# Optimization experiments

Hardware: AMD Instinct MI355X
Metric: run time of the kernel (lower is better)

## Reference

```python
import jax, jax.numpy as jnp
import numpy as np

N, E = 50000, 800000        # nodes, edges
L, MUL, S = 2, 32, 5        # layers, irrep multiplicity, num_species
NB, H = 8, 64               # num_bessel, radial MLP hidden
R_MAX = 5.0
AVG_NEIGH = 16.0
NW = 4 * MUL                # radial-MLP output size: 4 uvu TP paths x mul


def _envelope(x, p=6):
    # polynomial cutoff envelope u(x), smoothly -> 0 at x=1
    u = (1.0
         - (p + 1.0) * (p + 2.0) / 2.0 * x ** p
         + p * (p + 2.0) * x ** (p + 1)
         - p * (p + 1.0) / 2.0 * x ** (p + 2))
    return u * (x < 1.0)


def _forward(edge_vectors, node_species, senders, receivers, embed_w,
             w_res_s, w_res_v, w_lin1_s, w_lin1_v, mlp_w0, mlp_w1, mlp_w2,
             w_lin2_s, w_lin2_v, w_out1, w_out2):
    r = jnp.sqrt(jnp.sum(edge_vectors ** 2, -1) + 1e-12)            # [E] safe_norm
    unit = edge_vectors / r[:, None]
    sh1 = jnp.sqrt(3.0) * unit                                      # l=1 SH, component norm [E,3]
    # Bessel radial basis * polynomial envelope -> edge embedding [E,NB]
    n = jnp.arange(1, NB + 1, dtype=jnp.float32)
    bessel = jnp.sqrt(2.0 / R_MAX) * jnp.sin(n[None, :] * jnp.pi * r[:, None] / R_MAX) / r[:, None]
    edge_embedded = bessel * _envelope(r / R_MAX)[:, None]

    onehot = jax.nn.one_hot(node_species, S, dtype=jnp.float32)     # [N,S] node attrs (Sx0e)
    h_s = (onehot @ embed_w) / jnp.sqrt(S)                          # [N,MUL] 0e features
    h_v = jnp.zeros((N, MUL, 3), jnp.float32)                       # [N,MUL,3] 1o features (no path from 0e attrs)

    for l in range(L):
        # residual: FullyConnectedTensorProduct(node_feats, node_attrs) into h_out irreps
        res_s = jnp.einsum('nu,ns,usk->nk', h_s, onehot, w_res_s[l]) / jnp.sqrt(MUL * S)   # [N,2*MUL] (feat+gate scalars)
        res_v = jnp.einsum('nui,ns,usv->nvi', h_v, onehot, w_res_v[l]) / jnp.sqrt(MUL * S) # [N,MUL,3]
        # self-interaction Linear (per-irrep channel mixing)
        hs = (h_s @ w_lin1_s[l]) / jnp.sqrt(MUL)
        hv = jnp.einsum('nui,uv->nvi', h_v, w_lin1_v[l]) / jnp.sqrt(MUL)
        # gather sender node features onto edges
        es, ev = hs[senders], hv[senders]                           # [E,MUL], [E,MUL,3]
        # radial MLP (swish, no bias) -> per-edge uvu TP path weights [E, 4*MUL]
        a = jax.nn.silu(edge_embedded @ (mlp_w0[l] / jnp.sqrt(NB)))
        a = jax.nn.silu(a @ (mlp_w1[l] / jnp.sqrt(H)))
        w = a @ mlp_w2[l]
        w1, w2, w3, w4 = jnp.split(w, 4, axis=-1)
        # per-edge Clebsch-Gordan tensor product, uvu mode, radial weights
        o0a = w1 * es                                               # 0e x 0e -> 0e
        o0b = w2 * jnp.einsum('eui,ei->eu', ev, sh1) / jnp.sqrt(3.0)  # 1o x 1o -> 0e
        o1a = (w3 * es)[:, :, None] * sh1[:, None, :]               # 0e x 1o -> 1o
        o1b = w4[:, :, None] * ev                                   # 1o x 0e -> 1o
        # scatter-sum to receiver nodes + neighbor normalization
        seg = lambda x: jax.ops.segment_sum(x, receivers, num_segments=N) / AVG_NEIGH
        n0 = jnp.concatenate([seg(o0a), seg(o0b)], axis=-1)         # [N,2*MUL]
        n1 = jnp.concatenate([seg(o1a), seg(o1b)], axis=1)          # [N,2*MUL,3]
        # Linear to h_out irreps, add residual
        s_out = n0 @ w_lin2_s[l] / jnp.sqrt(2 * MUL) + res_s        # [N,2*MUL]
        v_out = jnp.einsum('nui,uv->nvi', n1, w_lin2_v[l]) / jnp.sqrt(2 * MUL) + res_v
        # gated nonlinearity: swish on even scalars, swish-activated gates scale vectors
        h_s = jax.nn.silu(s_out[:, :MUL])
        h_v = v_out * jax.nn.silu(s_out[:, MUL:])[:, :, None]
    # scalar readout: MUL -> MUL//2 -> 1 per node
    z = (h_s @ w_out1) / jnp.sqrt(MUL)
    e_node = (z @ w_out2) / jnp.sqrt(MUL // 2)
    return jnp.ravel(e_node)                                        # [N]


def setup_inputs():
    key = jax.random.key(0)
    ks = jax.random.split(key, 16)
    return {
        "edge_vectors": jax.random.normal(ks[0], (E, 3), jnp.float32) * 2.0,
        "node_species": jax.random.randint(ks[1], (N,), 0, S),
        "senders": jax.random.randint(ks[2], (E,), 0, N),
        "receivers": jax.random.randint(ks[3], (E,), 0, N),
        "embed_w": jax.random.normal(ks[4], (S, MUL), jnp.float32),
        "w_res_s": jax.random.normal(ks[5], (L, MUL, S, 2 * MUL), jnp.float32),
        "w_res_v": jax.random.normal(ks[6], (L, MUL, S, MUL), jnp.float32),
        "w_lin1_s": jax.random.normal(ks[7], (L, MUL, MUL), jnp.float32),
        "w_lin1_v": jax.random.normal(ks[8], (L, MUL, MUL), jnp.float32),
        "mlp_w0": jax.random.normal(ks[9], (L, NB, H), jnp.float32) * 4.0,
        "mlp_w1": jax.random.normal(ks[10], (L, H, H), jnp.float32) * 4.0,
        "mlp_w2": jax.random.normal(ks[11], (L, H, NW), jnp.float32) * 4.0 / np.sqrt(H),
        "w_lin2_s": jax.random.normal(ks[12], (L, 2 * MUL, 2 * MUL), jnp.float32),
        "w_lin2_v": jax.random.normal(ks[13], (L, 2 * MUL, MUL), jnp.float32),
        "w_out1": jax.random.normal(ks[14], (MUL, MUL // 2), jnp.float32),
        "w_out2": jax.random.normal(ks[15], (MUL // 2, 1), jnp.float32),
    }


def reference(edge_vectors, node_species, senders, receivers, embed_w,
              w_res_s, w_res_v, w_lin1_s, w_lin1_v, mlp_w0, mlp_w1, mlp_w2,
              w_lin2_s, w_lin2_v, w_out1, w_out2):
    return _forward(edge_vectors, node_species, senders, receivers, embed_w,
                    w_res_s, w_res_v, w_lin1_s, w_lin1_v, mlp_w0, mlp_w1, mlp_w2,
                    w_lin2_s, w_lin2_v, w_out1, w_out2)
```

## Files before the change

### kernel.cpp

```cpp
#include <hip/hip_runtime.h>
#include <math.h>

#define NN 50000
#define EE 800000
#define TB 4096

typedef float f32x2 __attribute__((ext_vector_type(2)));
typedef float f32x4  __attribute__((ext_vector_type(4)));

__device__ __forceinline__ float silu_f(float x) {
    return x / (1.f + __expf(-x));
}

__global__ __launch_bounds__(256) void k_table(
        const float* __restrict__ mlp_w0, const float* __restrict__ mlp_w1,
        const float* __restrict__ mlp_w2,
        const float* __restrict__ embed_w, const float* __restrict__ w_lin1_s,
        float* __restrict__ tab0, float* __restrict__ tab1, float* __restrict__ fs) {
    __shared__ float stage[4][128];
    int wv = threadIdx.x >> 6, lane = threadIdx.x & 63;
    int wid = blockIdx.x * 4 + wv;
    int widc = wid > 2 * TB + 1 ? 2 * TB + 1 : wid;
    int l = widc / (TB + 1);
    int bin = widc - l * (TB + 1);
    float* st = stage[wv];

    float r = 5.f * (float)bin / (float)TB;
    if (r < 1e-6f) r = 1e-6f;
    float ir = 1.f / r;
    float xx = r * 0.2f;
    float env = 0.f;
    if (xx < 1.f) {
        float x2 = xx * xx, x3 = x2 * xx, x6 = x3 * x3, x7 = x6 * xx, x8 = x7 * xx;
        env = 1.f - 28.f * x6 + 48.f * x7 - 21.f * x8;
    }
    float coef = 0.6324555320336759f * env * ir;
    const float w5 = 0.6283185307179586f;

    float p = 0.f;
#pragma unroll
    for (int k = 0; k < 8; ++k)
        p += coef * __sinf(w5 * (float)(k + 1) * r) * mlp_w0[l * 512 + k * 64 + lane];
    float a1 = silu_f(p * 0.35355339059327373f);
    st[lane] = a1;
    __syncthreads();
    float q = 0.f;
    for (int j = 0; j < 64; ++j) q += st[j] * mlp_w1[l * 4096 + j * 64 + lane];
    float a2 = silu_f(q * 0.125f);
    __syncthreads();
    st[lane] = a2;
    __syncthreads();
    float wlo = 0.f, whi = 0.f;
    for (int h = 0; h < 64; ++h) {
        float a = st[h];
        wlo += a * mlp_w2[l * 8192 + h * 128 + lane];
        whi += a * mlp_w2[l * 8192 + h * 128 + 64 + lane];
    }
    __syncthreads();
    st[lane] = wlo;
    st[64 + lane] = whi;
    __syncthreads();
    if (wid <= 2 * TB + 1 && lane < 16) {
        f32x4 o;
        if (l == 0) {
            o[0] = st[lane]; o[1] = st[64 + lane];
            o[2] = st[16 + lane]; o[3] = st[80 + lane];
            ((f32x4*)tab0)[bin * 16 + lane] = o;
        } else {
            o[0] = st[lane]; o[1] = st[32 + lane];
            o[2] = st[16 + lane]; o[3] = st[48 + lane];
            ((f32x4*)tab1)[bin * 16 + lane] = o;
        }
    }
    int ft = (wid - (2 * TB + 2)) * 64 + lane;
    if (wid >= 2 * TB + 2 && ft < 160) {
        int sp = ft >> 5, v = ft & 31;
        float acc = 0.f;
#pragma unroll
        for (int u = 0; u < 32; ++u) acc += embed_w[sp * 32 + u] * w_lin1_s[u * 32 + v];
        fs[ft] = acc * 0.4472135954999579f * 0.17677669529663687f;
    }
}

__global__ void k_hist(const int* __restrict__ recv, int* __restrict__ deg) {
    int e = blockIdx.x * 256 + threadIdx.x;
    if (e < EE) atomicAdd(&deg[recv[e]], 1);
}

__global__ void k_scan(const int* __restrict__ deg, int* __restrict__ row_start,
                       int* __restrict__ cursor) {
    __shared__ int part[256];
    int t = threadIdx.x;
    int lo = t * 196, hi = lo + 196 > NN ? NN : lo + 196;
    int s = 0;
    if (t < 255) {
        const int4* d4 = (const int4*)(deg + lo);
#pragma unroll 7
        for (int i = 0; i < 49; ++i) { int4 v = d4[i]; s += v.x + v.y + v.z + v.w; }
    } else {
        for (int i = lo; i < hi; ++i) s += deg[i];
    }
    part[t] = s;
    __syncthreads();
    for (int d = 1; d < 256; d <<= 1) {
        int add = (t >= d) ? part[t - d] : 0;
        __syncthreads();
        part[t] += add;
        __syncthreads();
    }
    int run = part[t] - s;
    for (int i = lo; i < hi; ++i) {
        row_start[i] = run;
        cursor[i] = run;
        run += deg[i];
    }
    if (t == 255) row_start[NN] = run;
}

__global__ void k_fill(const int* __restrict__ recv, const int* __restrict__ senders,
                       const int* __restrict__ species, const float* __restrict__ evec,
                       int* __restrict__ cursor,
                       int* __restrict__ csr_send, int* __restrict__ csr_recv,
                       float* __restrict__ ev4) {
    int e = blockIdx.x * 256 + threadIdx.x;
    if (e >= EE) return;
    int rv = recv[e];
    int p = atomicAdd(&cursor[rv], 1);
    int snd = senders[e];
    csr_send[p] = snd | (species[snd] << 24);
    csr_recv[p] = rv;
    float x = evec[e * 3 + 0], y = evec[e * 3 + 1], z = evec[e * 3 + 2];
    float r = sqrtf(x * x + y * y + z * z + 1e-12f);
    float ir = 1.f / r;
    const float s3 = 1.7320508075688772f;
    float xb = r * ((float)TB / 5.f);
    if (xb > (float)TB) xb = (float)TB;
    f32x4 o;
    o[0] = s3 * x * ir;
    o[1] = s3 * y * ir;
    o[2] = s3 * z * ir;
    o[3] = xb;
    *(f32x4*)(ev4 + (size_t)p * 4) = o;
}

#define WROWS 18
#define WSTRIDE 256
template<int L>
__global__ __launch_bounds__(256) void k_mega(
    const int* __restrict__ csr_send, const int* __restrict__ csr_recv,
    const float* __restrict__ ev4, const int* __restrict__ row_start,
    const float* __restrict__ fs, const float* __restrict__ feat,
    const float* __restrict__ tab,
    float* __restrict__ n0, float* __restrict__ n1) {
    __shared__ f32x4 accw4[WROWS * WSTRIDE / 4];
    __shared__ f32x4 lds_esh[256];
    __shared__ float lds_x[256];
    __shared__ int lds_wd[256];
    __shared__ int sh_base, sh_last;
    float* accw = (float*)accw4;

    int tid = threadIdx.x;
    int p0 = blockIdx.x * 256;
    int lane = tid & 63;
    int wv = tid >> 6;
    int c0 = lane & 15;
    int rg = lane >> 4;

    for (int i = tid; i < WROWS * WSTRIDE / 4; i += 256) accw4[i] = (f32x4)0.f;

    int sndp = csr_send[p0 + tid];
    int rv = csr_recv[p0 + tid];
    if (tid == 0)   sh_base = rv;
    if (tid == 255) sh_last = rv;
    {
        f32x4 g = *(const f32x4*)(ev4 + (size_t)(p0 + tid) * 4);
        f32x4 esh;
        esh[0] = g[0]; esh[1] = g[1]; esh[2] = g[2];
        esh[3] = __int_as_float(sndp);
        lds_esh[tid] = esh;
        lds_x[tid] = g[3];
    }
    __syncthreads();
    int node_base = sh_base;
    lds_wd[tid] = rv - node_base;

    const f32x4* tabv = (const f32x4*)tab;
    const f32x4* feat4 = (const f32x4*)feat;
    const float rs3 = 0.5773502691896258f;

    for (int t = 0; t < 4; ++t) {
        int tOff = wv * 64 + t * 16;

        f32x4 eshv[4], dv[4];
        int wr[4];
        float es0[4], es1[4];
#pragma unroll
        for (int j = 0; j < 4; ++j) {
            int idx = tOff + rg * 4 + j;
            eshv[j] = lds_esh[idx];
            wr[j] = lds_wd[idx];
            float xb = lds_x[idx];
            int bin = (int)xb;
            if (bin >= TB) bin = TB - 1;
            float fr = xb - (float)bin;
            f32x4 lo = tabv[bin * 16 + c0];
            f32x4 hi = tabv[bin * 16 + 16 + c0];
            dv[j] = lo + fr * (hi - lo);
            if (L == 0) {
                int sp = ((unsigned)__float_as_int(eshv[j][3])) >> 24;
                es0[j] = fs[sp * 32 + c0];
                es1[j] = fs[sp * 32 + 16 + c0];
            }
        }

#pragma unroll
        for (int b = 0; b < 2; ++b) {
            int u = b * 16 + c0;
            float s0 = 0.f, s1 = 0.f, s2 = 0.f, s3v = 0.f;
            int curw = wr[0];
            auto emit = [&](int wrow) {
                if (L == 0) {
                    if (wrow < WROWS) {
                        float* arow = accw + wrow * WSTRIDE;
                        atomicAdd(arow + u, s0);
                        atomicAdd(arow + 64 + u, s1);
                        atomicAdd(arow + 128 + u, s2);
                        atomicAdd(arow + 192 + u, s3v);
                    } else {
                        int rvn = node_base + wrow;
                        atomicAdd(n0 + (size_t)rvn * 64 + u, s0);
                        atomicAdd(n1 + (size_t)rvn * 192 + u, s1);
                        atomicAdd(n1 + (size_t)rvn * 192 + 64 + u, s2);
                        atomicAdd(n1 + (size_t)rvn * 192 + 128 + u, s3v);
                    }
                } else {
                    if (wrow < WROWS) {
                        float* arow = accw + wrow * WSTRIDE;
                        atomicAdd(arow + u, s0);
                        atomicAdd(arow + 32 + u, s1);
                    } else {
                        int rvn = node_base + wrow;
                        atomicAdd(n0 + (size_t)rvn * 64 + u, s0);
                        atomicAdd(n0 + (size_t)rvn * 64 + 32 + u, s1);
                    }
                }
            };
#pragma unroll
            for (int j = 0; j < 4; ++j) {
                int wrow = wr[j];
                if (j > 0 && wrow != curw) {
                    emit(curw);
                    s0 = s1 = s2 = s3v = 0.f;
                    curw = wrow;
                }
                f32x4 esh = eshv[j];
                float dA = dv[j][2 * b];
                float dB = dv[j][2 * b + 1];
                if (L == 0) {
                    float es = b ? es1[j] : es0[j];
                    float t3 = dB * es;
                    s0  += dA * es;
                    s1  += t3 * esh[0];
                    s2  += t3 * esh[1];
                    s3v += t3 * esh[2];
                } else {
                    int s = __float_as_int(esh[3]) & 0xFFFFFF;
                    f32x4 f4 = feat4[(size_t)s * 32 + u];
                    float dot = f4[1] * esh[0] + f4[2] * esh[1] + f4[3] * esh[2];
                    s0 += dA * f4[0];
                    s1 += dB * dot * rs3;
                }
            }
            {
                int pw = __shfl_xor(curw, 16);
                float t0 = __shfl_xor(s0, 16), t1 = __shfl_xor(s1, 16);
                float t2 = 0.f, t3m = 0.f;
                if (L == 0) { t2 = __shfl_xor(s2, 16); t3m = __shfl_xor(s3v, 16); }
                bool alive = true;
                if (pw == curw) {
                    s0 += t0; s1 += t1;
                    if (L == 0) { s2 += t2; s3v += t3m; }
                    if (lane & 16) alive = false;
                }
                if (alive) emit(curw);
            }
        }
    }
    __syncthreads();

    int span = sh_last - node_base;
    if (span > WROWS - 1) span = WROWS - 1;
    for (int wl = 0; wl <= span; ++wl) {
        int n = node_base + wl;
        float v = accw[wl * WSTRIDE + tid];
        bool interior = (row_start[n] >= p0) && (row_start[n + 1] <= p0 + 256);
        if (L == 1) {
            if (tid < 64) {
                float* dest = n0 + (size_t)n * 64 + tid;
                if (interior) *dest = v;
                else if (v != 0.f) atomicAdd(dest, v);
            }
        } else {
            float* dest = (tid < 64) ? (n0 + (size_t)n * 64 + tid) : (n1 + (size_t)n * 192 + (tid - 64));
            if (interior) *dest = v;
            else if (v != 0.f) atomicAdd(dest, v);
        }
    }
}

__global__ __launch_bounds__(256) void k_upd0_prep(
        const int* __restrict__ species,
        const float* __restrict__ n0, const float* __restrict__ n1,
        const float* __restrict__ w_lin2_s, const float* __restrict__ w_lin2_v,
        const float* __restrict__ w_res_s, const float* __restrict__ embed_w,
        const float* __restrict__ w_lin1_s, const float* __restrict__ w_lin1_v,
        float* __restrict__ h_s, float* __restrict__ feat) {
    __shared__ float stage[4][128];
    int lane = threadIdx.x & 63;
    int wv = threadIdx.x >> 6;
    int n = blockIdx.x * 4 + wv;
    n = __builtin_amdgcn_readfirstlane(n);
    int sp = __builtin_amdgcn_readfirstlane(species[n]);
    const float sc_l2 = 1.f / 128.f;
    const float rr = 0.07905694150420949f * 0.4472135954999579f;

    const float* n0r = n0 + (size_t)n * 64;
    float sk = 0.f;
#pragma unroll 8
    for (int j = 0; j < 64; ++j)
        sk += n0r[j] * w_lin2_s[j * 64 + lane];
    sk *= sc_l2;
#pragma unroll 8
    for (int u = 0; u < 32; ++u)
        sk += (embed_w[sp * 32 + u] * rr) * w_res_s[(u * 5 + sp) * 64 + lane];
    float act = silu_f(sk);
    float gmine = __shfl(act, 32 + (lane & 31));

    const float* n1r = n1 + (size_t)n * 192;
    int i0 = lane >> 5, v = lane & 31;
    float acc0 = 0.f, acc2 = 0.f;
#pragma unroll 8
    for (int u = 0; u < 32; ++u) {
        float wlv = w_lin2_v[u * 32 + v];
        acc0 += n1r[i0 * 64 + u] * wlv;
        acc2 += n1r[128 + u] * wlv;
    }
    float* st = stage[wv];
    st[32 + i0 * 32 + v] = acc0 * sc_l2 * gmine;
    if (lane < 32) {
        st[v] = act;
        st[96 + v] = acc2 * sc_l2 * gmine;
        h_s[(size_t)n * 32 + v] = act;
    }
    __syncthreads();

    const float rs32 = 0.17677669529663687f;
    float accA = 0.f, accB = 0.f;
#pragma unroll 8
    for (int u = 0; u < 32; ++u) {
        float wsv = w_lin1_s[u * 32 + v];
        float wvv = w_lin1_v[u * 32 + v];
        float xs = st[u];
        float xx = st[32 + u];
        float xy = st[64 + u];
        float xz = st[96 + u];
        float inA = i0 ? xy : xs;
        float wA  = i0 ? wvv : wsv;
        float inB = i0 ? xz : xx;
        accA += inA * wA;
        accB += inB * wvv;
    }
    f32x2 o;
    o[0] = accA * rs32;
    o[1] = accB * rs32;
    *(f32x2*)(feat + (size_t)n * 128 + v * 4 + i0 * 2) = o;
}

__global__ __launch_bounds__(256) void k_node_update_last(
        const int* __restrict__ species,
        const float* __restrict__ n0,
        const float* __restrict__ w_lin2_s, const float* __restrict__ w_res_s,
        const float* __restrict__ h_s,
        const float* __restrict__ w_out1, const float* __restrict__ w_out2,
        float* __restrict__ out) {
    int lane = threadIdx.x & 63;
    int n = blockIdx.x * 4 + (threadIdx.x >> 6);
    n = __builtin_amdgcn_readfirstlane(n);
    if (lane >= 32) return;
    int sp = __builtin_amdgcn_readfirstlane(species[n]);
    const float sc_l2 = 1.f / 128.f;
    const float rs160 = 0.07905694150420949f;

    const float* n0r = n0 + (size_t)n * 64;
    float sk = 0.f;
#pragma unroll 8
    for (int j = 0; j < 64; ++j)
        sk += n0r[j] * w_lin2_s[j * 64 + lane];
    sk *= sc_l2;
    const float* hsr = h_s + (size_t)n * 32;
#pragma unroll 8
    for (int u = 0; u < 32; ++u)
        sk += (hsr[u] * rs160) * w_res_s[(u * 5 + sp) * 64 + lane];
    float act = silu_f(sk);

    float wc = 0.f;
#pragma unroll
    for (int j = 0; j < 16; ++j)
        wc += w_out1[lane * 16 + j] * w_out2[j];
    float e = act * wc;
    e += __shfl_xor(e, 1);
    e += __shfl_xor(e, 2);
    e += __shfl_xor(e, 4);
    e += __shfl_xor(e, 8);
    e += __shfl_xor(e, 16);
    if (lane == 0)
        out[n] = e * 0.17677669529663687f * 0.25f;
}

extern "C" void kernel_launch(void* const* d_in, const int* in_sizes, int n_in,
                              void* d_out, int out_size, void* d_ws, size_t ws_size,
                              hipStream_t stream) {
    const float* evec     = (const float*)d_in[0];
    const int*   species  = (const int*)d_in[1];
    const int*   senders  = (const int*)d_in[2];
    const int*   receivers= (const int*)d_in[3];
    const float* embed_w  = (const float*)d_in[4];
    const float* w_res_s  = (const float*)d_in[5];
    const float* w_res_v  = (const float*)d_in[6];
    const float* w_lin1_s = (const float*)d_in[7];
    const float* w_lin1_v = (const float*)d_in[8];
    const float* mlp_w0   = (const float*)d_in[9];
    const float* mlp_w1   = (const float*)d_in[10];
    const float* mlp_w2   = (const float*)d_in[11];
    const float* w_lin2_s = (const float*)d_in[12];
    const float* w_lin2_v = (const float*)d_in[13];
    const float* w_out1   = (const float*)d_in[14];
    const float* w_out2   = (const float*)d_in[15];
    (void)w_res_v;

    float* ws = (float*)d_ws;
    size_t off = 0;
    auto alloc = [&](size_t n) { float* p = ws + off; off += (n + 3) & ~(size_t)3; return p; };

    float* h_s  = alloc(NN * 32);
    float* feat = alloc((size_t)NN * 128);
    float* n0b  = alloc(NN * 64);
    float* n1b  = alloc(NN * 192);
    int*   deg  = (int*)alloc(NN);
    float* tab0 = alloc((size_t)(TB + 1) * 64);
    float* tab1 = alloc((size_t)(TB + 1) * 64);
    float* fs   = alloc(160);
    int*   row_start = (int*)alloc(NN + 1);
    int*   cursor    = (int*)alloc(NN);
    int*   csr_send  = (int*)alloc(EE);
    int*   csr_recv  = (int*)alloc(EE);
    float* ev4       = alloc((size_t)EE * 4);

    hipMemsetAsync(n0b, 0, (size_t)NN * 257 * 4, stream);
    k_table<<<(2 * (TB + 1) + 3 + 3) / 4, 256, 0, stream>>>(
        mlp_w0, mlp_w1, mlp_w2, embed_w, w_lin1_s, tab0, tab1, fs);
    k_hist<<<(EE + 255) / 256, 256, 0, stream>>>(receivers, deg);
    k_scan<<<1, 256, 0, stream>>>(deg, row_start, cursor);
    k_fill<<<(EE + 255) / 256, 256, 0, stream>>>(receivers, senders, species, evec,
                                                 cursor, csr_send, csr_recv, ev4);

    k_mega<0><<<EE / 256, 256, 0, stream>>>(
        csr_send, csr_recv, ev4, row_start, fs, feat, tab0, n0b, n1b);
    k_upd0_prep<<<12500, 256, 0, stream>>>(
        species, n0b, n1b, w_lin2_s, w_lin2_v, w_res_s, embed_w,
        w_lin1_s + 1024, w_lin1_v + 1024, h_s, feat);

    hipMemsetAsync(n0b, 0, (size_t)NN * 64 * 4, stream);
    k_mega<1><<<EE / 256, 256, 0, stream>>>(
        csr_send, csr_recv, ev4, row_start, fs, feat, tab1, n0b, n1b);
    k_node_update_last<<<12500, 256, 0, stream>>>(
        species, n0b, w_lin2_s + 4096, w_res_s + 10240, h_s,
        w_out1, w_out2, (float*)d_out);
}
```

Baseline: 559.0 us.

## Widen scan to 1024 threads and streamline edge aggregation in mega kernel

The single-block CSR scan now runs with 1024 threads, each summing 49 degrees, so the serial per-thread loop is shorter. In the message kernel the LDS staging of edge data is dropped: each lane reads ev4, csr_send and csr_recv straight from global memory, and node_base comes from readfirstlane. A second xor-32 shuffle merges partial sums across half-waves before emitting LDS atomics, reducing atomic traffic. The accumulator is padded (stride 260, 20 rows), only the used columns are zeroed, and results are written back as float4 with fewer idle threads, at the cost of redundant global loads and more shuffles.

```diff
diff --git a/kernel.cpp b/kernel.cpp
--- a/kernel.cpp
+++ b/kernel.cpp
@@ -87,22 +87,19 @@
     if (e < EE) atomicAdd(&deg[recv[e]], 1);
 }
 
-__global__ void k_scan(const int* __restrict__ deg, int* __restrict__ row_start,
-                       int* __restrict__ cursor) {
-    __shared__ int part[256];
+__global__ __launch_bounds__(1024) void k_scan(
+        const int* __restrict__ deg, int* __restrict__ row_start,
+        int* __restrict__ cursor) {
+    __shared__ int part[1024];
     int t = threadIdx.x;
-    int lo = t * 196, hi = lo + 196 > NN ? NN : lo + 196;
+    int lo = t * 49, hi = lo + 49;
+    if (hi > NN) hi = NN;
+    if (lo > NN) lo = NN;
     int s = 0;
-    if (t < 255) {
-        const int4* d4 = (const int4*)(deg + lo);
-#pragma unroll 7
-        for (int i = 0; i < 49; ++i) { int4 v = d4[i]; s += v.x + v.y + v.z + v.w; }
-    } else {
-        for (int i = lo; i < hi; ++i) s += deg[i];
-    }
+    for (int i = lo; i < hi; ++i) s += deg[i];
     part[t] = s;
     __syncthreads();
-    for (int d = 1; d < 256; d <<= 1) {
+    for (int d = 1; d < 1024; d <<= 1) {
         int add = (t >= d) ? part[t - d] : 0;
         __syncthreads();
         part[t] += add;
@@ -114,7 +111,7 @@
         cursor[i] = run;
         run += deg[i];
     }
-    if (t == 255) row_start[NN] = run;
+    if (t == 1023) row_start[NN] = run;
 }
 
 __global__ void k_fill(const int* __restrict__ recv, const int* __restrict__ senders,
@@ -143,8 +140,8 @@
     *(f32x4*)(ev4 + (size_t)p * 4) = o;
 }
 
-#define WROWS 18
-#define WSTRIDE 256
+#define WROWS 20
+#define WSTRIDE 260
 template<int L>
 __global__ __launch_bounds__(256) void k_mega(
     const int* __restrict__ csr_send, const int* __restrict__ csr_recv,
@@ -152,13 +149,7 @@
     const float* __restrict__ fs, const float* __restrict__ feat,
     const float* __restrict__ tab,
     float* __restrict__ n0, float* __restrict__ n1) {
-    __shared__ f32x4 accw4[WROWS * WSTRIDE / 4];
-    __shared__ f32x4 lds_esh[256];
-    __shared__ float lds_x[256];
-    __shared__ int lds_wd[256];
-    __shared__ int sh_base, sh_last;
-    float* accw = (float*)accw4;
-
+    __shared__ float accw[WROWS * WSTRIDE];
     int tid = threadIdx.x;
     int p0 = blockIdx.x * 256;
     int lane = tid & 63;
@@ -166,23 +157,16 @@
     int c0 = lane & 15;
     int rg = lane >> 4;
 
-    for (int i = tid; i < WROWS * WSTRIDE / 4; i += 256) accw4[i] = (f32x4)0.f;
-
-    int sndp = csr_send[p0 + tid];
-    int rv = csr_recv[p0 + tid];
-    if (tid == 0)   sh_base = rv;
-    if (tid == 255) sh_last = rv;
-    {
-        f32x4 g = *(const f32x4*)(ev4 + (size_t)(p0 + tid) * 4);
-        f32x4 esh;
-        esh[0] = g[0]; esh[1] = g[1]; esh[2] = g[2];
-        esh[3] = __int_as_float(sndp);
-        lds_esh[tid] = esh;
-        lds_x[tid] = g[3];
-    }
-    __syncthreads();
-    int node_base = sh_base;
-    lds_wd[tid] = rv - node_base;
+    int node_base = __builtin_amdgcn_readfirstlane(csr_recv[p0]);
+    int last_rv   = __builtin_amdgcn_readfirstlane(csr_recv[p0 + 255]);
+
+    const int NCH4 = (L == 0) ? 32 : 16;
+    for (int i = tid; i < WROWS * NCH4; i += 256) {
+        int row = i / NCH4, k = i - row * NCH4;
+        int chunk = (L == 0) ? ((k >> 3) * 16 + (k & 7)) : k;
+        *(f32x4*)&accw[row * WSTRIDE + chunk * 4] = (f32x4)0.f;
+    }
+    __syncthreads();
 
     const f32x4* tabv = (const f32x4*)tab;
     const f32x4* feat4 = (const f32x4*)feat;
@@ -190,16 +174,17 @@
 
     for (int t = 0; t < 4; ++t) {
         int tOff = wv * 64 + t * 16;
-
         f32x4 eshv[4], dv[4];
-        int wr[4];
+        int wr[4], snd[4];
         float es0[4], es1[4];
 #pragma unroll
         for (int j = 0; j < 4; ++j) {
-            int idx = tOff + rg * 4 + j;
-            eshv[j] = lds_esh[idx];
-            wr[j] = lds_wd[idx];
-            float xb = lds_x[idx];
+            int gidx = p0 + tOff + rg * 4 + j;
+            f32x4 g = *(const f32x4*)(ev4 + (size_t)gidx * 4);
+            snd[j] = csr_send[gidx];
+            wr[j] = csr_recv[gidx] - node_base;
+            eshv[j] = g;
+            float xb = g[3];
             int bin = (int)xb;
             if (bin >= TB) bin = TB - 1;
             float fr = xb - (float)bin;
@@ -207,9 +192,9 @@
             f32x4 hi = tabv[bin * 16 + 16 + c0];
             dv[j] = lo + fr * (hi - lo);
             if (L == 0) {
-                int sp = ((unsigned)__float_as_int(eshv[j][3])) >> 24;
-                es0[j] = fs[sp * 32 + c0];
-                es1[j] = fs[sp * 32 + 16 + c0];
+                int spp = ((unsigned)snd[j]) >> 24;
+                es0[j] = fs[spp * 32 + c0];
+                es1[j] = fs[spp * 32 + 16 + c0];
             }
         }
 
@@ -264,46 +249,85 @@
                     s2  += t3 * esh[1];
                     s3v += t3 * esh[2];
                 } else {
-                    int s = __float_as_int(esh[3]) & 0xFFFFFF;
+                    int s = snd[j] & 0xFFFFFF;
                     f32x4 f4 = feat4[(size_t)s * 32 + u];
                     float dot = f4[1] * esh[0] + f4[2] * esh[1] + f4[3] * esh[2];
                     s0 += dA * f4[0];
                     s1 += dB * dot * rs3;
                 }
             }
+            int alive = 1;
             {
                 int pw = __shfl_xor(curw, 16);
                 float t0 = __shfl_xor(s0, 16), t1 = __shfl_xor(s1, 16);
                 float t2 = 0.f, t3m = 0.f;
                 if (L == 0) { t2 = __shfl_xor(s2, 16); t3m = __shfl_xor(s3v, 16); }
-                bool alive = true;
                 if (pw == curw) {
                     s0 += t0; s1 += t1;
                     if (L == 0) { s2 += t2; s3v += t3m; }
-                    if (lane & 16) alive = false;
+                    if (lane & 16) alive = 0;
                 }
-                if (alive) emit(curw);
+            }
+            {
+                int pw = __shfl_xor(curw, 32);
+                int pal = __shfl_xor(alive, 32);
+                float t0 = __shfl_xor(s0, 32), t1 = __shfl_xor(s1, 32);
+                float t2 = 0.f, t3m = 0.f;
+                if (L == 0) { t2 = __shfl_xor(s2, 32); t3m = __shfl_xor(s3v, 32); }
+                if (alive && pal && pw == curw) {
+                    s0 += t0; s1 += t1;
+                    if (L == 0) { s2 += t2; s3v += t3m; }
+                    if (lane & 32) alive = 0;
+                }
+            }
+            if (alive) emit(curw);
+        }
+    }
+    __syncthreads();
+
+    int span = last_rv - node_base;
+    if (span > WROWS - 1) span = WROWS - 1;
+    if (L == 0) {
+        int rsub = tid >> 5;
+        int k = tid & 31;
+        int chunk = (k >> 3) * 16 + (k & 7);
+        int seg = k >> 3;
+        int u4 = (k & 7) * 4;
+        for (int wl0 = 0; wl0 <= span; wl0 += 8) {
+            int wl = wl0 + rsub;
+            if (wl > span) continue;
+            int n = node_base + wl;
+            f32x4 v = *(f32x4*)&accw[wl * WSTRIDE + chunk * 4];
+            bool interior = (row_start[n] >= p0) && (row_start[n + 1] <= p0 + 256);
+            float* dest = (seg == 0) ? (n0 + (size_t)n * 64 + u4)
+                                     : (n1 + (size_t)n * 192 + (seg - 1) * 64 + u4);
+            if (interior) {
+                *(f32x4*)dest = v;
+            } else {
+                if (v[0] != 0.f) atomicAdd(dest + 0, v[0]);
+                if (v[1] != 0.f) atomicAdd(dest + 1, v[1]);
+                if (v[2] != 0.f) atomicAdd(dest + 2, v[2]);
+                if (v[3] != 0.f) atomicAdd(dest + 3, v[3]);
             }
         }
-    }
-    __syncthreads();
-
-    int span = sh_last - node_base;
-    if (span > WROWS - 1) span = WROWS - 1;
-    for (int wl = 0; wl <= span; ++wl) {
-        int n = node_base + wl;
-        float v = accw[wl * WSTRIDE + tid];
-        bool interior = (row_start[n] >= p0) && (row_start[n + 1] <= p0 + 256);
-        if (L == 1) {
-            if (tid < 64) {
-                float* dest = n0 + (size_t)n * 64 + tid;
-                if (interior) *dest = v;
-                else if (v != 0.f) atomicAdd(dest, v);
+    } else {
+        int rsub = tid >> 4;
+        int k = tid & 15;
+        for (int wl0 = 0; wl0 <= span; wl0 += 16) {
+            int wl = wl0 + rsub;
+            if (wl > span) continue;
+            int n = node_base + wl;
+            f32x4 v = *(f32x4*)&accw[wl * WSTRIDE + k * 4];
+            bool interior = (row_start[n] >= p0) && (row_start[n + 1] <= p0 + 256);
+            float* dest = n0 + (size_t)n * 64 + k * 4;
+            if (interior) {
+                *(f32x4*)dest = v;
+            } else {
+                if (v[0] != 0.f) atomicAdd(dest + 0, v[0]);
+                if (v[1] != 0.f) atomicAdd(dest + 1, v[1]);
+                if (v[2] != 0.f) atomicAdd(dest + 2, v[2]);
+                if (v[3] != 0.f) atomicAdd(dest + 3, v[3]);
             }
-        } else {
-            float* dest = (tid < 64) ? (n0 + (size_t)n * 64 + tid) : (n1 + (size_t)n * 192 + (tid - 64));
-            if (interior) *dest = v;
-            else if (v != 0.f) atomicAdd(dest, v);
         }
     }
 }
@@ -460,7 +484,7 @@
     k_table<<<(2 * (TB + 1) + 3 + 3) / 4, 256, 0, stream>>>(
         mlp_w0, mlp_w1, mlp_w2, embed_w, w_lin1_s, tab0, tab1, fs);
     k_hist<<<(EE + 255) / 256, 256, 0, stream>>>(receivers, deg);
-    k_scan<<<1, 256, 0, stream>>>(deg, row_start, cursor);
+    k_scan<<<1, 1024, 0, stream>>>(deg, row_start, cursor);
     k_fill<<<(EE + 255) / 256, 256, 0, stream>>>(receivers, senders, species, evec,
                                                  cursor, csr_send, csr_recv, ev4);
 
```

New measurement: 551.7 us (median of 2 runs). Within noise of the previous version (-1.3%).
